# Optimization experiments

Measured on AMD Instinct MI355X. Metric: run time of the kernel, lower is better.

## Reference

```python
import jax, jax.numpy as jnp
import numpy as np

N, C, T, V = 8, 256, 256, 25
NH = 8
DK = 256           # dk_factor(1.0) * out_channels
DV = 256           # only_temporal_attention -> dv = out_channels
DKH = DK // NH     # 32
DVH = DV // NH     # 32
BN_EPS = 1e-5


def setup_inputs() -> dict:
    key = jax.random.key(0)
    ks = jax.random.split(key, 10)
    return {
        "x": jax.random.normal(ks[0], (N, C, T, V), jnp.float32),
        # pointwise (1,1) qkv conv: weight (2*dk+dv, C), torch conv_init scale
        "qkv_w": jax.random.normal(ks[1], (2 * DK + DV, C), jnp.float32) * (2.0 / (2 * DK + DV)) ** 0.5,
        "qkv_b": jax.random.normal(ks[2], (2 * DK + DV,), jnp.float32) * 0.02,
        # relative key embeddings: (2*frames-1, dk // Nh)
        "key_rel": jax.random.normal(ks[3], (2 * T - 1, DKH), jnp.float32),
        # attn_out pointwise conv: (dv, dv)
        "attn_w": jax.random.normal(ks[4], (DV, DV), jnp.float32) * (1.0 / DV) ** 0.5,
        "attn_b": jax.random.normal(ks[5], (DV,), jnp.float32) * 0.02,
        # BatchNorm2d (eval mode) params / running stats
        "bn_gamma": 1.0 + 0.1 * jax.random.normal(ks[6], (DV,), jnp.float32),
        "bn_beta": 0.1 * jax.random.normal(ks[7], (DV,), jnp.float32),
        "bn_mean": 0.1 * jax.random.normal(ks[8], (DV,), jnp.float32),
        "bn_var": jax.random.uniform(ks[9], (DV,), jnp.float32, minval=0.5, maxval=1.5),
    }


def rel_to_abs(x):
    # x: (B, Nh, L, 2L-1) -> (B, Nh, L, L) via standard pad/reshape/slice trick
    B, Nh, L, _ = x.shape
    x = jnp.pad(x, ((0, 0), (0, 0), (0, 0), (0, 1)))          # (B,Nh,L,2L)
    flat = x.reshape(B, Nh, L * 2 * L)
    flat = jnp.pad(flat, ((0, 0), (0, 0), (0, L - 1)))
    final = flat.reshape(B, Nh, L + 1, 2 * L - 1)
    return final[:, :, :L, L - 1:]


def reference(x, qkv_w, qkv_b, key_rel, attn_w, attn_b, bn_gamma, bn_beta, bn_mean, bn_var):
    n, c, t, v = x.shape
    x_sum = x
    B = n * v
    # (N,C,T,V) -> (N*V, C, T): each joint is an independent temporal sequence
    xr = jnp.transpose(x, (0, 3, 1, 2)).reshape(B, c, t)
    # pointwise qkv conv (kernel (1,1), stride 1)
    qkv = jnp.einsum('bct,oc->bot', xr, qkv_w) + qkv_b[None, :, None]
    q, k, vv = qkv[:, :DK], qkv[:, DK:2 * DK], qkv[:, 2 * DK:]
    q = q.reshape(B, NH, DKH, t) * (DKH ** -0.5)   # scaling applied before rel logits too
    k = k.reshape(B, NH, DKH, t)
    vv = vv.reshape(B, NH, DVH, t)
    # content logits: (B,NH,t,t)
    logits = jnp.einsum('bhdt,bhds->bhts', q, k)
    # relative logits: (B,NH,t,2t-1) -> abs (B,NH,t,t)
    rel = jnp.einsum('bhdt,md->bhtm', q, key_rel)
    logits = logits + rel_to_abs(rel)
    weights = jax.nn.softmax(logits, axis=-1)
    attn = jnp.einsum('bhts,bhds->bhtd', weights, vv)          # (B,NH,t,DVH)
    # combine heads (head-major channel order) -> (B, DV, t)
    attn = jnp.transpose(attn, (0, 1, 3, 2)).reshape(B, DV, t)
    # attn_out pointwise conv
    attn = jnp.einsum('bct,oc->bot', attn, attn_w) + attn_b[None, :, None]
    # (N*V, DV, T) -> (N, DV, T, V)
    attn = attn.reshape(n, v, DV, t).transpose(0, 2, 3, 1)
    # skip connection (in==out, stride==1 -> identity down path)
    result = attn + x_sum
    # BatchNorm2d in eval mode
    inv = bn_gamma / jnp.sqrt(bn_var + BN_EPS)
    result = result * inv[None, :, None, None] + (bn_beta - bn_mean * inv)[None, :, None, None]
    return jax.nn.relu(result)
```

## Files before the change

kernel.cpp:

```cpp
#include <hip/hip_runtime.h>

#define NB 8
#define CC 256
#define TT 256
#define VV 25

typedef unsigned int u32;
typedef unsigned short u16;
typedef __attribute__((ext_vector_type(8))) short s16x8;
typedef __attribute__((ext_vector_type(4))) float f32x4;

__device__ __forceinline__ float bf2f(u16 u) { return __uint_as_float((u32)u << 16); }
__device__ __forceinline__ u16 f2bf(float f) {
    u32 u = __float_as_uint(f);
    u += 0x7fffu + ((u >> 16) & 1u);
    return (u16)(u >> 16);
}
__device__ __forceinline__ u16 f2bf_rtz(float f) { return (u16)(__float_as_uint(f) >> 16); }

__device__ __forceinline__ void gload_lds16(const void* g, void* l) {
    __builtin_amdgcn_global_load_lds(
        (const __attribute__((address_space(1))) u32*)g,
        (__attribute__((address_space(3))) u32*)l, 16, 0, 0);
}

__global__ __launch_bounds__(256) void k_transpose_x(const float* __restrict__ x,
                                                     u16* __restrict__ xT) {
    __shared__ u16 L[25 * 32 * 34];
    const int tid = threadIdx.x;
    const int c0 = blockIdx.x * 32;
    const int t0 = blockIdx.y * 32;
    const int n  = blockIdx.z;
    for (int i = tid; i < 25600; i += 256) {
        int ci = i / 800;
        int rem = i - ci * 800;
        int t = rem / 25;
        int v = rem - t * 25;
        float f = x[(((size_t)(n * CC + c0 + ci)) * TT + t0) * VV + rem];
        L[(v * 32 + t) * 34 + ci] = f2bf(f);
    }
    __syncthreads();
    for (int i = tid; i < 12800; i += 256) {
        int row = i >> 4, cp = i & 15;
        int v = row >> 5, t = row & 31;
        u32 val = *(const u32*)&L[row * 34 + cp * 2];
        *(u32*)&xT[(((size_t)(n * VV + v)) * TT + t0 + t) * CC + c0 + cp * 2] = val;
    }
}

__global__ __launch_bounds__(256) void k_pack_all(const float* __restrict__ qkv_w,
                                                  const float* __restrict__ attn_w,
                                                  const float* __restrict__ qkv_b,
                                                  const float* __restrict__ key_rel,
                                                  u16* __restrict__ Wqk,
                                                  u16* __restrict__ Wv,
                                                  u16* __restrict__ Wo,
                                                  float* __restrict__ bqk,
                                                  u16* __restrict__ krb) {
    const float s = 0.17677669529663687f;
    int g = blockIdx.x * 256 + threadIdx.x;
    if (g < 131072) {
        Wqk[g] = f2bf(qkv_w[g] * (g < 65536 ? s : 1.f));
    } else if (g < 196608) {
        Wv[g - 131072] = f2bf(qkv_w[g]);
    } else if (g < 262144) {
        Wo[g - 196608] = f2bf(attn_w[g - 196608]);
    } else if (g < 262656) {
        int i = g - 262144;
        bqk[i] = qkv_b[i] * (i < 256 ? s : 1.f);
    } else if (g < 279040) {
        int i = g - 262656;
        krb[i] = (i < 511 * 32) ? f2bf(key_rel[i]) : (u16)0;
    }
}

__device__ __forceinline__ void gemm_mainloop(const u16* __restrict__ Arow,
                                              const u16* __restrict__ Brow,
                                              u16* At, u16* Bt,
                                              int wave, int lane, f32x4 acc[4][4]) {
    const int srow = lane >> 2, scol = (lane & 3) * 8;
    const int quad = lane >> 4, l15 = lane & 15;
    for (int k0 = 0; k0 < 256; k0 += 32) {
#pragma unroll
        for (int it = 0; it < 2; ++it) {
            int ch = it * 4 + wave;
            gload_lds16(Arow + (size_t)(ch * 16 + srow) * 256 + k0 + scol, At + ch * 512 + lane * 8);
            gload_lds16(Brow + (size_t)(ch * 16 + srow) * 256 + k0 + scol, Bt + ch * 512 + lane * 8);
        }
        __syncthreads();
        s16x8 af[4], bfr[4];
#pragma unroll
        for (int i = 0; i < 4; ++i)
            af[i] = *(const s16x8*)&At[((wave & 1) * 64 + i * 16 + l15) * 32 + quad * 8];
#pragma unroll
        for (int j = 0; j < 4; ++j)
            bfr[j] = *(const s16x8*)&Bt[((wave >> 1) * 64 + j * 16 + l15) * 32 + quad * 8];
#pragma unroll
        for (int i = 0; i < 4; ++i)
#pragma unroll
            for (int j = 0; j < 4; ++j)
                acc[i][j] = __builtin_amdgcn_mfma_f32_16x16x32_bf16(af[i], bfr[j], acc[i][j], 0, 0, 0);
        __syncthreads();
    }
}

__global__ __launch_bounds__(256) void k_gemm_qk(const u16* __restrict__ xT,
                                                 const u16* __restrict__ Wqk,
                                                 const float* __restrict__ bqk,
                                                 u16* __restrict__ qk_all) {
    __shared__ __align__(16) u16 At[128 * 32];
    __shared__ __align__(16) u16 Bt[128 * 32];
    const int tid = threadIdx.x, wave = tid >> 6, lane = tid & 63;
    const int quad = lane >> 4, l15 = lane & 15;
    const int n0 = blockIdx.x * 128;
    const int m0 = blockIdx.y * 128;
    const int b  = blockIdx.z;
    const u16* Arow = xT + (size_t)b * 65536 + (size_t)m0 * 256;
    const u16* Brow = Wqk + (size_t)n0 * 256;
    f32x4 acc[4][4];
#pragma unroll
    for (int i = 0; i < 4; ++i)
#pragma unroll
        for (int j = 0; j < 4; ++j) acc[i][j] = (f32x4){0.f, 0.f, 0.f, 0.f};
    gemm_mainloop(Arow, Brow, At, Bt, wave, lane, acc);

    u16* ob = qk_all + (size_t)b * 131072;
    const int nb = n0 + (wave >> 1) * 64 + l15;
    float bj[4];
#pragma unroll
    for (int j = 0; j < 4; ++j) bj[j] = bqk[nb + j * 16];
#pragma unroll
    for (int i = 0; i < 4; ++i) {
        int t_i = m0 + (wave & 1) * 64 + i * 16 + quad * 4;
#pragma unroll
        for (int r = 0; r < 4; ++r) {
            u16* orow = ob + (size_t)(t_i + r) * 512 + nb;
#pragma unroll
            for (int j = 0; j < 4; ++j)
                orow[j * 16] = f2bf(acc[i][j][r] + bj[j]);
        }
    }
}

__global__ __launch_bounds__(256) void k_gemm_av(const u16* __restrict__ Wb,
                                                 const float* __restrict__ bias,
                                                 const u16* __restrict__ Bsrc,
                                                 u16* __restrict__ Out) {
    __shared__ __align__(16) u16 At[128 * 32];
    __shared__ __align__(16) u16 Bt[128 * 32];
    const int tid = threadIdx.x, wave = tid >> 6, lane = tid & 63;
    const int quad = lane >> 4, l15 = lane & 15;
    const int n0 = blockIdx.x * 128;
    const int m0 = blockIdx.y * 128;
    const int b  = blockIdx.z;
    const u16* Arow = Wb + (size_t)m0 * 256;
    const u16* Brow = Bsrc + (size_t)b * 65536 + (size_t)n0 * 256;
    f32x4 acc[4][4];
#pragma unroll
    for (int i = 0; i < 4; ++i)
#pragma unroll
        for (int j = 0; j < 4; ++j) acc[i][j] = (f32x4){0.f, 0.f, 0.f, 0.f};
    gemm_mainloop(Arow, Brow, At, Bt, wave, lane, acc);

    u16* ob = Out + (size_t)b * 65536;
    const int nb = n0 + (wave >> 1) * 64 + l15;
#pragma unroll
    for (int i = 0; i < 4; ++i) {
        int o_i = m0 + (wave & 1) * 64 + i * 16 + quad * 4;
#pragma unroll
        for (int r = 0; r < 4; ++r) {
            float bv = bias[o_i + r];
            u16* orow = ob + (size_t)(o_i + r) * 256 + nb;
#pragma unroll
            for (int j = 0; j < 4; ++j)
                orow[j * 16] = f2bf(acc[i][j][r] + bv);
        }
    }
}

__global__ __launch_bounds__(256, 3) void k_attention_mfma(const u16* __restrict__ qk,
                                                           const u16* __restrict__ vb,
                                                           const u16* __restrict__ krb,
                                                           u16* __restrict__ attn) {
    __shared__ __align__(16) u16 RP[4][16 * 280];

    const int tid = threadIdx.x;
    const int L = blockIdx.x;
    const int b = (L & 7) * 25 + ((L >> 3) % 25);
    const int h = L / 200;
    const int bh = b * 8 + h;
    const int wave = tid >> 6, lane = tid & 63;
    const int quad = lane >> 4, l15 = lane & 15;
    const int t0w = blockIdx.y * 64 + wave * 16;
    const int tl = quad * 4;

    u16* rp = &RP[wave][0];
    const u16* qrow = qk + (size_t)b * 131072;
    const u16* vg   = vb + (size_t)bh * 8192;
    const u16* krg  = krb + (size_t)(240 - t0w) * 32;

    s16x8 afrag = *(const s16x8*)(qrow + (size_t)(t0w + l15) * 512 + h * 32 + quad * 8);

    s16x8 krf[17];
#pragma unroll
    for (int j = 0; j < 17; ++j)
        krf[j] = *(const s16x8*)(krg + (size_t)(j * 16 + l15) * 32 + quad * 8);
#pragma unroll
    for (int j = 0; j < 17; ++j) {
        f32x4 c = {0.f, 0.f, 0.f, 0.f};
        c = __builtin_amdgcn_mfma_f32_16x16x32_bf16(afrag, krf[j], c, 0, 0, 0);
        int col = j * 16 + l15;
        rp[(tl + 0) * 280 + col] = f2bf_rtz(c[0]);
        rp[(tl + 1) * 280 + col] = f2bf_rtz(c[1]);
        rp[(tl + 2) * 280 + col] = f2bf_rtz(c[2]);
        rp[(tl + 3) * 280 + col] = f2bf_rtz(c[3]);
    }

    s16x8 kf[16];
#pragma unroll
    for (int n = 0; n < 16; ++n)
        kf[n] = *(const s16x8*)(qrow + (size_t)(n * 16 + l15) * 512 + 256 + h * 32 + quad * 8);
    f32x4 acc[16];
#pragma unroll
    for (int n = 0; n < 16; ++n) {
#pragma unroll
        for (int r = 0; r < 4; ++r) {
            int tlr = tl + r;
            acc[n][r] = bf2f(rp[tlr * 280 + (n * 16 + l15 - tlr + 15)]);
        }
    }
#pragma unroll
    for (int n = 0; n < 16; ++n)
        acc[n] = __builtin_amdgcn_mfma_f32_16x16x32_bf16(afrag, kf[n], acc[n], 0, 0, 0);

    float invr[4];
#pragma unroll
    for (int r = 0; r < 4; ++r) {
        float tmp[16];
#pragma unroll
        for (int n = 0; n < 16; ++n) tmp[n] = acc[n][r];
#pragma unroll
        for (int st = 8; st; st >>= 1)
#pragma unroll
            for (int n = 0; n < 8; ++n)
                if (n < st) tmp[n] = fmaxf(tmp[n], tmp[n + st]);
        float m = tmp[0];
#pragma unroll
        for (int off = 1; off < 16; off <<= 1) m = fmaxf(m, __shfl_xor(m, off, 64));
        float sm[16];
#pragma unroll
        for (int n = 0; n < 16; ++n) {
            float e = __expf(acc[n][r] - m);
            acc[n][r] = e;
            sm[n] = e;
        }
#pragma unroll
        for (int st = 8; st; st >>= 1)
#pragma unroll
            for (int n = 0; n < 8; ++n)
                if (n < st) sm[n] += sm[n + st];
        float s = sm[0];
#pragma unroll
        for (int off = 1; off < 16; off <<= 1) s += __shfl_xor(s, off, 64);
        invr[r] = 1.f / s;
    }
#pragma unroll
    for (int n = 0; n < 16; ++n) {
#pragma unroll
        for (int r = 0; r < 4; ++r)
            rp[(tl + r) * 280 + n * 16 + l15] = f2bf_rtz(acc[n][r] * invr[r]);
    }

#pragma unroll
    for (int j = 0; j < 2; ++j) {
        s16x8 vf[8], pa[8];
#pragma unroll
        for (int ks = 0; ks < 8; ++ks)
            vf[ks] = *(const s16x8*)(vg + (size_t)(j * 16 + l15) * 256 + ks * 32 + quad * 8);
#pragma unroll
        for (int ks = 0; ks < 8; ++ks)
            pa[ks] = *(const s16x8*)&rp[l15 * 280 + ks * 32 + quad * 8];
        f32x4 o0 = {0.f, 0.f, 0.f, 0.f}, o1 = {0.f, 0.f, 0.f, 0.f};
#pragma unroll
        for (int ks = 0; ks < 8; ks += 2) {
            o0 = __builtin_amdgcn_mfma_f32_16x16x32_bf16(pa[ks],     vf[ks],     o0, 0, 0, 0);
            o1 = __builtin_amdgcn_mfma_f32_16x16x32_bf16(pa[ks + 1], vf[ks + 1], o1, 0, 0, 0);
        }
        u16* ob = attn + ((size_t)b * 256 + t0w + tl) * 256 + h * 32 + j * 16 + l15;
        ob[0]   = f2bf(o0[0] + o1[0]);
        ob[256] = f2bf(o0[1] + o1[1]);
        ob[512] = f2bf(o0[2] + o1[2]);
        ob[768] = f2bf(o0[3] + o1[3]);
    }
}

__global__ __launch_bounds__(256) void k_final(const u16* __restrict__ y,
                                               const float* __restrict__ x,
                                               const float* __restrict__ gamma,
                                               const float* __restrict__ beta,
                                               const float* __restrict__ mean,
                                               const float* __restrict__ var,
                                               float* __restrict__ out) {
    __shared__ float tile[1600];
    const int tid = threadIdx.x;
    const int t0 = blockIdx.x * 64;
    const int o  = blockIdx.y;
    const int n  = blockIdx.z;
    float inv = gamma[o] * rsqrtf(var[o] + 1e-5f);
    float sh  = beta[o] - mean[o] * inv;
    for (int p = tid; p < 1600; p += 256) {
        int v = p >> 6, j = p & 63;
        tile[j * VV + v] = bf2f(y[(((size_t)(n * VV + v)) * CC + o) * TT + t0 + j]);
    }
    __syncthreads();
    size_t gbase = (((size_t)(n * CC + o)) * TT + t0) * VV;
    for (int i = tid; i < 1600; i += 256) {
        float val = tile[i] + x[gbase + i];
        val = val * inv + sh;
        out[gbase + i] = fmaxf(val, 0.f);
    }
}

extern "C" void kernel_launch(void* const* d_in, const int* in_sizes, int n_in,
                              void* d_out, int out_size, void* d_ws, size_t ws_size,
                              hipStream_t stream) {
    const float* x        = (const float*)d_in[0];
    const float* qkv_w    = (const float*)d_in[1];
    const float* qkv_b    = (const float*)d_in[2];
    const float* key_rel  = (const float*)d_in[3];
    const float* attn_w   = (const float*)d_in[4];
    const float* attn_b   = (const float*)d_in[5];
    const float* bn_gamma = (const float*)d_in[6];
    const float* bn_beta  = (const float*)d_in[7];
    const float* bn_mean  = (const float*)d_in[8];
    const float* bn_var   = (const float*)d_in[9];
    float* out = (float*)d_out;

    char* ws = (char*)d_ws;
    u16* xT     = (u16*)ws;
    u16* qk_all = (u16*)(ws + 26214400);
    u16* vb     = (u16*)(ws + 78643200);
    u16* attnT  = (u16*)(ws + 104857600);
    u16* y      = qk_all;

    char* outc = (char*)d_out;
    u16* Wqk   = (u16*)outc;
    u16* Wv    = (u16*)(outc + 262144);
    u16* Wo    = (u16*)(outc + 393216);
    float* bqk = (float*)(outc + 524288);
    u16* krb   = (u16*)(outc + 526336);

    k_pack_all<<<1090, 256, 0, stream>>>(qkv_w, attn_w, qkv_b, key_rel, Wqk, Wv, Wo, bqk, krb);
    k_transpose_x<<<dim3(8, 8, 8), 256, 0, stream>>>(x, xT);
    k_gemm_qk<<<dim3(4, 2, 200), 256, 0, stream>>>(xT, Wqk, bqk, qk_all);
    k_gemm_av<<<dim3(2, 2, 200), 256, 0, stream>>>(Wv, qkv_b + 512, xT, vb);
    k_attention_mfma<<<dim3(1600, 4), 256, 0, stream>>>(qk_all, vb, krb, attnT);
    k_gemm_av<<<dim3(2, 2, 200), 256, 0, stream>>>(Wo, attn_b, attnT, y);
    k_final<<<dim3(4, 256, 8), 256, 0, stream>>>(y, x, bn_gamma, bn_beta, bn_mean, bn_var, out);
}
```

Before: 360.3 us.

## Fuse QKV GEMMs and fold output projection with residual, BN, ReLU

Merges the QK and V projection GEMMs into one launch by dispatching on blockIdx.x. The attention kernel now writes its output in (N, T, V, C) order, so the output-projection GEMM can treat each batch's T*V positions as columns. That GEMM epilogue applies the bias, residual add, precomputed BN scale and shift, and ReLU, writing fp32 output directly. This removes the intermediate bf16 y buffer, the separate k_final transpose kernel, and one launch. The trade-offs are strided attention stores and less-coalesced x and out accesses in the GEMM epilogue, since each lane hits 16-column chunks of rows 6400 elements long.

```diff
diff --git a/kernel.cpp b/kernel.cpp
--- a/kernel.cpp
+++ b/kernel.cpp
@@ -52,11 +52,16 @@
                                                   const float* __restrict__ attn_w,
                                                   const float* __restrict__ qkv_b,
                                                   const float* __restrict__ key_rel,
+                                                  const float* __restrict__ bn_gamma,
+                                                  const float* __restrict__ bn_beta,
+                                                  const float* __restrict__ bn_mean,
+                                                  const float* __restrict__ bn_var,
                                                   u16* __restrict__ Wqk,
                                                   u16* __restrict__ Wv,
                                                   u16* __restrict__ Wo,
                                                   float* __restrict__ bqk,
-                                                  u16* __restrict__ krb) {
+                                                  u16* __restrict__ krb,
+                                                  float* __restrict__ bnis) {
     const float s = 0.17677669529663687f;
     int g = blockIdx.x * 256 + threadIdx.x;
     if (g < 131072) {
@@ -71,6 +76,15 @@
     } else if (g < 279040) {
         int i = g - 262656;
         krb[i] = (i < 511 * 32) ? f2bf(key_rel[i]) : (u16)0;
+    } else if (g < 279552) {
+        int i = g - 279040;
+        if (i < 256) {
+            bnis[i] = bn_gamma[i] * rsqrtf(bn_var[i] + 1e-5f);
+        } else {
+            int o = i - 256;
+            float iv = bn_gamma[o] * rsqrtf(bn_var[o] + 1e-5f);
+            bnis[i] = bn_beta[o] - bn_mean[o] * iv;
+        }
     }
 }
 
@@ -104,19 +118,25 @@
     }
 }
 
-__global__ __launch_bounds__(256) void k_gemm_qk(const u16* __restrict__ xT,
-                                                 const u16* __restrict__ Wqk,
-                                                 const float* __restrict__ bqk,
-                                                 u16* __restrict__ qk_all) {
+__global__ __launch_bounds__(256) void k_gemm_qkv(const u16* __restrict__ xT,
+                                                  const u16* __restrict__ Wqk,
+                                                  const u16* __restrict__ Wv,
+                                                  const float* __restrict__ bqk,
+                                                  const float* __restrict__ qkv_b,
+                                                  u16* __restrict__ qk_all,
+                                                  u16* __restrict__ vb) {
     __shared__ __align__(16) u16 At[128 * 32];
     __shared__ __align__(16) u16 Bt[128 * 32];
     const int tid = threadIdx.x, wave = tid >> 6, lane = tid & 63;
     const int quad = lane >> 4, l15 = lane & 15;
-    const int n0 = blockIdx.x * 128;
-    const int m0 = blockIdx.y * 128;
+    const int bx = blockIdx.x;
     const int b  = blockIdx.z;
-    const u16* Arow = xT + (size_t)b * 65536 + (size_t)m0 * 256;
-    const u16* Brow = Wqk + (size_t)n0 * 256;
+    const bool isv = (bx >= 4);
+    const int n0 = (isv ? blockIdx.y : bx) * 128;
+    const int m0 = (isv ? (bx - 4) : (int)blockIdx.y) * 128;
+    const u16* xb = xT + (size_t)b * 65536;
+    const u16* Arow = isv ? (Wv + (size_t)m0 * 256) : (xb + (size_t)m0 * 256);
+    const u16* Brow = isv ? (xb + (size_t)n0 * 256) : (Wqk + (size_t)n0 * 256);
     f32x4 acc[4][4];
 #pragma unroll
     for (int i = 0; i < 4; ++i)
@@ -124,56 +144,36 @@
         for (int j = 0; j < 4; ++j) acc[i][j] = (f32x4){0.f, 0.f, 0.f, 0.f};
     gemm_mainloop(Arow, Brow, At, Bt, wave, lane, acc);
 
-    u16* ob = qk_all + (size_t)b * 131072;
     const int nb = n0 + (wave >> 1) * 64 + l15;
-    float bj[4];
-#pragma unroll
-    for (int j = 0; j < 4; ++j) bj[j] = bqk[nb + j * 16];
-#pragma unroll
-    for (int i = 0; i < 4; ++i) {
-        int t_i = m0 + (wave & 1) * 64 + i * 16 + quad * 4;
-#pragma unroll
-        for (int r = 0; r < 4; ++r) {
-            u16* orow = ob + (size_t)(t_i + r) * 512 + nb;
-#pragma unroll
-            for (int j = 0; j < 4; ++j)
-                orow[j * 16] = f2bf(acc[i][j][r] + bj[j]);
-        }
-    }
-}
-
-__global__ __launch_bounds__(256) void k_gemm_av(const u16* __restrict__ Wb,
-                                                 const float* __restrict__ bias,
-                                                 const u16* __restrict__ Bsrc,
-                                                 u16* __restrict__ Out) {
-    __shared__ __align__(16) u16 At[128 * 32];
-    __shared__ __align__(16) u16 Bt[128 * 32];
-    const int tid = threadIdx.x, wave = tid >> 6, lane = tid & 63;
-    const int quad = lane >> 4, l15 = lane & 15;
-    const int n0 = blockIdx.x * 128;
-    const int m0 = blockIdx.y * 128;
-    const int b  = blockIdx.z;
-    const u16* Arow = Wb + (size_t)m0 * 256;
-    const u16* Brow = Bsrc + (size_t)b * 65536 + (size_t)n0 * 256;
-    f32x4 acc[4][4];
-#pragma unroll
-    for (int i = 0; i < 4; ++i)
-#pragma unroll
-        for (int j = 0; j < 4; ++j) acc[i][j] = (f32x4){0.f, 0.f, 0.f, 0.f};
-    gemm_mainloop(Arow, Brow, At, Bt, wave, lane, acc);
-
-    u16* ob = Out + (size_t)b * 65536;
-    const int nb = n0 + (wave >> 1) * 64 + l15;
-#pragma unroll
-    for (int i = 0; i < 4; ++i) {
-        int o_i = m0 + (wave & 1) * 64 + i * 16 + quad * 4;
-#pragma unroll
-        for (int r = 0; r < 4; ++r) {
-            float bv = bias[o_i + r];
-            u16* orow = ob + (size_t)(o_i + r) * 256 + nb;
-#pragma unroll
-            for (int j = 0; j < 4; ++j)
-                orow[j * 16] = f2bf(acc[i][j][r] + bv);
+    if (!isv) {
+        u16* ob = qk_all + (size_t)b * 131072;
+        float bj[4];
+#pragma unroll
+        for (int j = 0; j < 4; ++j) bj[j] = bqk[nb + j * 16];
+#pragma unroll
+        for (int i = 0; i < 4; ++i) {
+            int t_i = m0 + (wave & 1) * 64 + i * 16 + quad * 4;
+#pragma unroll
+            for (int r = 0; r < 4; ++r) {
+                u16* orow = ob + (size_t)(t_i + r) * 512 + nb;
+#pragma unroll
+                for (int j = 0; j < 4; ++j)
+                    orow[j * 16] = f2bf(acc[i][j][r] + bj[j]);
+            }
+        }
+    } else {
+        u16* ob = vb + (size_t)b * 65536;
+#pragma unroll
+        for (int i = 0; i < 4; ++i) {
+            int o_i = m0 + (wave & 1) * 64 + i * 16 + quad * 4;
+#pragma unroll
+            for (int r = 0; r < 4; ++r) {
+                float bv = qkv_b[512 + o_i + r];
+                u16* orow = ob + (size_t)(o_i + r) * 256 + nb;
+#pragma unroll
+                for (int j = 0; j < 4; ++j)
+                    orow[j * 16] = f2bf(acc[i][j][r] + bv);
+            }
         }
     }
 }
@@ -181,12 +181,14 @@
 __global__ __launch_bounds__(256, 3) void k_attention_mfma(const u16* __restrict__ qk,
                                                            const u16* __restrict__ vb,
                                                            const u16* __restrict__ krb,
-                                                           u16* __restrict__ attn) {
+                                                           u16* __restrict__ attnF) {
     __shared__ __align__(16) u16 RP[4][16 * 280];
 
     const int tid = threadIdx.x;
     const int L = blockIdx.x;
-    const int b = (L & 7) * 25 + ((L >> 3) % 25);
+    const int n = L & 7;
+    const int v = (L >> 3) % 25;
+    const int b = n * 25 + v;
     const int h = L / 200;
     const int bh = b * 8 + h;
     const int wave = tid >> 6, lane = tid & 63;
@@ -218,57 +220,57 @@
 
     s16x8 kf[16];
 #pragma unroll
-    for (int n = 0; n < 16; ++n)
-        kf[n] = *(const s16x8*)(qrow + (size_t)(n * 16 + l15) * 512 + 256 + h * 32 + quad * 8);
+    for (int nn = 0; nn < 16; ++nn)
+        kf[nn] = *(const s16x8*)(qrow + (size_t)(nn * 16 + l15) * 512 + 256 + h * 32 + quad * 8);
     f32x4 acc[16];
 #pragma unroll
-    for (int n = 0; n < 16; ++n) {
+    for (int nn = 0; nn < 16; ++nn) {
 #pragma unroll
         for (int r = 0; r < 4; ++r) {
             int tlr = tl + r;
-            acc[n][r] = bf2f(rp[tlr * 280 + (n * 16 + l15 - tlr + 15)]);
-        }
-    }
-#pragma unroll
-    for (int n = 0; n < 16; ++n)
-        acc[n] = __builtin_amdgcn_mfma_f32_16x16x32_bf16(afrag, kf[n], acc[n], 0, 0, 0);
+            acc[nn][r] = bf2f(rp[tlr * 280 + (nn * 16 + l15 - tlr + 15)]);
+        }
+    }
+#pragma unroll
+    for (int nn = 0; nn < 16; ++nn)
+        acc[nn] = __builtin_amdgcn_mfma_f32_16x16x32_bf16(afrag, kf[nn], acc[nn], 0, 0, 0);
 
     float invr[4];
 #pragma unroll
     for (int r = 0; r < 4; ++r) {
         float tmp[16];
 #pragma unroll
-        for (int n = 0; n < 16; ++n) tmp[n] = acc[n][r];
+        for (int nn = 0; nn < 16; ++nn) tmp[nn] = acc[nn][r];
 #pragma unroll
         for (int st = 8; st; st >>= 1)
 #pragma unroll
-            for (int n = 0; n < 8; ++n)
-                if (n < st) tmp[n] = fmaxf(tmp[n], tmp[n + st]);
+            for (int nn = 0; nn < 8; ++nn)
+                if (nn < st) tmp[nn] = fmaxf(tmp[nn], tmp[nn + st]);
         float m = tmp[0];
 #pragma unroll
         for (int off = 1; off < 16; off <<= 1) m = fmaxf(m, __shfl_xor(m, off, 64));
         float sm[16];
 #pragma unroll
-        for (int n = 0; n < 16; ++n) {
-            float e = __expf(acc[n][r] - m);
-            acc[n][r] = e;
-            sm[n] = e;
+        for (int nn = 0; nn < 16; ++nn) {
+            float e = __expf(acc[nn][r] - m);
+            acc[nn][r] = e;
+            sm[nn] = e;
         }
 #pragma unroll
         for (int st = 8; st; st >>= 1)
 #pragma unroll
-            for (int n = 0; n < 8; ++n)
-                if (n < st) sm[n] += sm[n + st];
+            for (int nn = 0; nn < 8; ++nn)
+                if (nn < st) sm[nn] += sm[nn + st];
         float s = sm[0];
 #pragma unroll
         for (int off = 1; off < 16; off <<= 1) s += __shfl_xor(s, off, 64);
         invr[r] = 1.f / s;
     }
 #pragma unroll
-    for (int n = 0; n < 16; ++n) {
+    for (int nn = 0; nn < 16; ++nn) {
 #pragma unroll
         for (int r = 0; r < 4; ++r)
-            rp[(tl + r) * 280 + n * 16 + l15] = f2bf_rtz(acc[n][r] * invr[r]);
+            rp[(tl + r) * 280 + nn * 16 + l15] = f2bf_rtz(acc[nn][r] * invr[r]);
     }
 
 #pragma unroll
@@ -286,38 +288,55 @@
             o0 = __builtin_amdgcn_mfma_f32_16x16x32_bf16(pa[ks],     vf[ks],     o0, 0, 0, 0);
             o1 = __builtin_amdgcn_mfma_f32_16x16x32_bf16(pa[ks + 1], vf[ks + 1], o1, 0, 0, 0);
         }
-        u16* ob = attn + ((size_t)b * 256 + t0w + tl) * 256 + h * 32 + j * 16 + l15;
-        ob[0]   = f2bf(o0[0] + o1[0]);
-        ob[256] = f2bf(o0[1] + o1[1]);
-        ob[512] = f2bf(o0[2] + o1[2]);
-        ob[768] = f2bf(o0[3] + o1[3]);
-    }
-}
-
-__global__ __launch_bounds__(256) void k_final(const u16* __restrict__ y,
-                                               const float* __restrict__ x,
-                                               const float* __restrict__ gamma,
-                                               const float* __restrict__ beta,
-                                               const float* __restrict__ mean,
-                                               const float* __restrict__ var,
-                                               float* __restrict__ out) {
-    __shared__ float tile[1600];
-    const int tid = threadIdx.x;
-    const int t0 = blockIdx.x * 64;
-    const int o  = blockIdx.y;
+        u16* ob = attnF + (((size_t)(n * 256 + t0w + tl)) * 25 + v) * 256 + h * 32 + j * 16 + l15;
+        ob[0]        = f2bf(o0[0] + o1[0]);
+        ob[6400]     = f2bf(o0[1] + o1[1]);
+        ob[12800]    = f2bf(o0[2] + o1[2]);
+        ob[19200]    = f2bf(o0[3] + o1[3]);
+    }
+}
+
+__global__ __launch_bounds__(256) void k_gemm_out(const u16* __restrict__ Wo,
+                                                  const float* __restrict__ attn_b,
+                                                  const u16* __restrict__ attnF,
+                                                  const float* __restrict__ x,
+                                                  const float* __restrict__ bnis,
+                                                  float* __restrict__ out) {
+    __shared__ __align__(16) u16 At[128 * 32];
+    __shared__ __align__(16) u16 Bt[128 * 32];
+    const int tid = threadIdx.x, wave = tid >> 6, lane = tid & 63;
+    const int quad = lane >> 4, l15 = lane & 15;
+    const int n0 = blockIdx.x * 128;
+    const int m0 = blockIdx.y * 128;
     const int n  = blockIdx.z;
-    float inv = gamma[o] * rsqrtf(var[o] + 1e-5f);
-    float sh  = beta[o] - mean[o] * inv;
-    for (int p = tid; p < 1600; p += 256) {
-        int v = p >> 6, j = p & 63;
-        tile[j * VV + v] = bf2f(y[(((size_t)(n * VV + v)) * CC + o) * TT + t0 + j]);
-    }
-    __syncthreads();
-    size_t gbase = (((size_t)(n * CC + o)) * TT + t0) * VV;
-    for (int i = tid; i < 1600; i += 256) {
-        float val = tile[i] + x[gbase + i];
-        val = val * inv + sh;
-        out[gbase + i] = fmaxf(val, 0.f);
+    const u16* Arow = Wo + (size_t)m0 * 256;
+    const u16* Brow = attnF + (size_t)n * 6400 * 256 + (size_t)n0 * 256;
+    f32x4 acc[4][4];
+#pragma unroll
+    for (int i = 0; i < 4; ++i)
+#pragma unroll
+        for (int j = 0; j < 4; ++j) acc[i][j] = (f32x4){0.f, 0.f, 0.f, 0.f};
+    gemm_mainloop(Arow, Brow, At, Bt, wave, lane, acc);
+
+    const int nb = n0 + (wave >> 1) * 64 + l15;
+#pragma unroll
+    for (int i = 0; i < 4; ++i) {
+        int o_i = m0 + (wave & 1) * 64 + i * 16 + quad * 4;
+#pragma unroll
+        for (int r = 0; r < 4; ++r) {
+            int o = o_i + r;
+            float ab = attn_b[o];
+            float iv = bnis[o];
+            float sh = bnis[256 + o];
+            const float* xrow = x + ((size_t)(n * 256 + o)) * 6400;
+            float* orow = out + ((size_t)(n * 256 + o)) * 6400;
+#pragma unroll
+            for (int j = 0; j < 4; ++j) {
+                int col = nb + j * 16;
+                float val = (acc[i][j][r] + ab + xrow[col]) * iv + sh;
+                orow[col] = fmaxf(val, 0.f);
+            }
+        }
     }
 }
 
@@ -338,23 +357,22 @@
 
     char* ws = (char*)d_ws;
     u16* xT     = (u16*)ws;
+    u16* attnF  = (u16*)ws;
     u16* qk_all = (u16*)(ws + 26214400);
     u16* vb     = (u16*)(ws + 78643200);
-    u16* attnT  = (u16*)(ws + 104857600);
-    u16* y      = qk_all;
-
-    char* outc = (char*)d_out;
-    u16* Wqk   = (u16*)outc;
-    u16* Wv    = (u16*)(outc + 262144);
-    u16* Wo    = (u16*)(outc + 393216);
-    float* bqk = (float*)(outc + 524288);
-    u16* krb   = (u16*)(outc + 526336);
-
-    k_pack_all<<<1090, 256, 0, stream>>>(qkv_w, attn_w, qkv_b, key_rel, Wqk, Wv, Wo, bqk, krb);
+    char* wsc   = ws + 104857600;
+    u16* Wqk    = (u16*)wsc;
+    u16* Wv     = (u16*)(wsc + 262144);
+    u16* Wo     = (u16*)(wsc + 393216);
+    float* bqk  = (float*)(wsc + 524288);
+    u16* krb    = (u16*)(wsc + 526336);
+    float* bnis = (float*)(wsc + 559104);
+
+    k_pack_all<<<1092, 256, 0, stream>>>(qkv_w, attn_w, qkv_b, key_rel,
+                                         bn_gamma, bn_beta, bn_mean, bn_var,
+                                         Wqk, Wv, Wo, bqk, krb, bnis);
     k_transpose_x<<<dim3(8, 8, 8), 256, 0, stream>>>(x, xT);
-    k_gemm_qk<<<dim3(4, 2, 200), 256, 0, stream>>>(xT, Wqk, bqk, qk_all);
-    k_gemm_av<<<dim3(2, 2, 200), 256, 0, stream>>>(Wv, qkv_b + 512, xT, vb);
-    k_attention_mfma<<<dim3(1600, 4), 256, 0, stream>>>(qk_all, vb, krb, attnT);
-    k_gemm_av<<<dim3(2, 2, 200), 256, 0, stream>>>(Wo, attn_b, attnT, y);
-    k_final<<<dim3(4, 256, 8), 256, 0, stream>>>(y, x, bn_gamma, bn_beta, bn_mean, bn_var, out);
-}
+    k_gemm_qkv<<<dim3(6, 2, 200), 256, 0, stream>>>(xT, Wqk, Wv, bqk, qkv_b, qk_all, vb);
+    k_attention_mfma<<<dim3(1600, 4), 256, 0, stream>>>(qk_all, vb, krb, attnF);
+    k_gemm_out<<<dim3(50, 2, 8), 256, 0, stream>>>(Wo, attn_b, attnF, x, bnis, out);
+}
```

After: 352.8 us. 1.02x faster.
